# Kernel optimization log

Measured on AMD Instinct MI355X. Metric: run time of the kernel, lower is better.

The kernel has to match this reference:

```python
import jax, jax.numpy as jnp
import numpy as np

# DCT-III (a.k.a. IDCT), unnormalized, scaled to match the DREAMPlace kernel:
#   y_k = x_0 + 2 * sum_{n=1}^{N-1} x_n * cos(pi * n * (2k+1) / (2N))
# (the docstring's Re{1/2 x0 + sum xn e^{j pi n (2k+1)/(2N)}} scaled by 2).
# Computed in O(N log N) via a length-2N FFT:
#   y_k = Re{ sum_n c_n x_n e^{j pi n/(2N)} e^{2 pi j n k/(2N)} }
# which is 2N * ifft(pad(a, 2N)) evaluated at k = 0..N-1, with
#   a_n = c_n * x_n * exp(j pi n / (2N)),  c_0 = 1, c_{n>0} = 2.

def _idct_last_dim(x):
    N = x.shape[-1]
    n = jnp.arange(N)
    c = jnp.where(n == 0, 1.0, 2.0).astype(x.dtype)
    twiddle = jnp.exp(1j * (jnp.pi / (2 * N)) * n.astype(jnp.float32)).astype(jnp.complex64)
    a = (c * x).astype(jnp.complex64) * twiddle          # [.., N]
    y = jnp.fft.ifft(a, n=2 * N, axis=-1)                # [.., 2N]
    return (y.real[..., :N] * (2 * N)).astype(x.dtype)


def setup_inputs() -> dict:
    key = jax.random.key(0)
    x = jax.random.normal(key, (4096, 4096), dtype=jnp.float32)
    return {"x": x}


def reference(x) -> jnp.ndarray:
    return _idct_last_dim(x)
```

## Files before the change

kernel.cpp:

```cpp
#include <hip/hip_runtime.h>
#include <cstdint>


#define NN 4096
#define HH 2048
#define BM 128
#define BN 128
#define BK 128

typedef int i32x4 __attribute__((ext_vector_type(4)));
typedef int i32x2 __attribute__((ext_vector_type(2)));

__device__ __forceinline__ void async_copy16(void* lds_base, const void* gptr) {
    __builtin_amdgcn_global_load_lds(
        (const __attribute__((address_space(1))) unsigned int*)gptr,
        (__attribute__((address_space(3))) unsigned int*)lds_base,
        16, 0, 0);
}

__device__ __forceinline__ int pack4(int q0, int q1, int q2, int q3) {
    return (q0 & 255) | ((q1 & 255) << 8) | ((q2 & 255) << 16) | ((q3 & 255) << 24);
}

__global__ __launch_bounds__(256) void prep_i8(const float* __restrict__ x,
                                               signed char* __restrict__ Ae,
                                               signed char* __restrict__ Ao,
                                               signed char* __restrict__ CEm,
                                               signed char* __restrict__ COm,
                                               float* __restrict__ se,
                                               float* __restrict__ so) {
    const int b = blockIdx.x;
    const int t = threadIdx.x;
    const float s = 3.834951969714103e-4f;

    if (b < 4096) {
        __shared__ float rede[256], redo[256];
        const float* xr = x + (size_t)b * NN;
        float v[16];
#pragma unroll
        for (int j = 0; j < 4; ++j) {
            float4 f = ((const float4*)xr)[t * 4 + j];
            v[j * 4 + 0] = f.x; v[j * 4 + 1] = f.y;
            v[j * 4 + 2] = f.z; v[j * 4 + 3] = f.w;
        }
        float emax = 1e-30f, omax = 1e-30f;
#pragma unroll
        for (int i = 0; i < 8; ++i) {
            emax = fmaxf(emax, __builtin_fabsf(v[2 * i]));
            omax = fmaxf(omax, __builtin_fabsf(v[2 * i + 1]));
        }
        rede[t] = emax; redo[t] = omax;
        __syncthreads();
        for (int sr = 128; sr > 0; sr >>= 1) {
            if (t < sr) {
                rede[t] = fmaxf(rede[t], rede[t + sr]);
                redo[t] = fmaxf(redo[t], redo[t + sr]);
            }
            __syncthreads();
        }
        const float rmax_e = rede[0], rmax_o = redo[0];
        const float inv_e = 127.0f / rmax_e, inv_o = 127.0f / rmax_o;
        int qe[8], qo[8];
#pragma unroll
        for (int i = 0; i < 8; ++i) {
            qe[i] = (int)rintf(v[2 * i] * inv_e);
            qo[i] = (int)rintf(v[2 * i + 1] * inv_o);
        }
        i32x2 oe, oo;
        oe[0] = pack4(qe[0], qe[1], qe[2], qe[3]);
        oe[1] = pack4(qe[4], qe[5], qe[6], qe[7]);
        oo[0] = pack4(qo[0], qo[1], qo[2], qo[3]);
        oo[1] = pack4(qo[4], qo[5], qo[6], qo[7]);
        ((i32x2*)(Ae + (size_t)b * HH))[t] = oe;
        ((i32x2*)(Ao + (size_t)b * HH))[t] = oo;
        if (t == 0) {
            se[b] = rmax_e * (1.0f / 127.0f);
            so[b] = rmax_o * (1.0f / 127.0f);
        }
    } else if (b < 6144) {
        const int k = b - 4096;
        const int twok1 = 2 * k + 1;
        int q[8];
#pragma unroll
        for (int i = 0; i < 8; ++i) {
            int m = t * 8 + i;
            int p = (2 * m * twok1) & 16383;
            float w = (m == 0) ? 1.0f : 2.0f;
            q[i] = (int)rintf(w * __cosf((float)p * s) * 63.5f);
        }
        i32x2 o;
        o[0] = pack4(q[0], q[1], q[2], q[3]);
        o[1] = pack4(q[4], q[5], q[6], q[7]);
        ((i32x2*)(CEm + (size_t)k * HH))[t] = o;
    } else {
        const int k = b - 6144;
        const int twok1 = 2 * k + 1;
        int q[8];
#pragma unroll
        for (int i = 0; i < 8; ++i) {
            int m = t * 8 + i;
            int p = ((2 * m + 1) * twok1) & 16383;
            q[i] = (int)rintf(__cosf((float)p * s) * 127.0f);
        }
        i32x2 o;
        o[0] = pack4(q[0], q[1], q[2], q[3]);
        o[1] = pack4(q[4], q[5], q[6], q[7]);
        ((i32x2*)(COm + (size_t)k * HH))[t] = o;
    }
}

__device__ __forceinline__ void gemm_pass(const signed char* __restrict__ A,
                                          const signed char* __restrict__ B,
                                          signed char* sA, signed char* sB,
                                          int rowBase, int colBase,
                                          int wave, int lane,
                                          i32x4 (&acc)[4][4]) {
    const int waveM = wave >> 1;
    const int waveN = wave & 1;
    const int srow  = lane >> 3;
    const int sgran = lane & 7;
    const int ggcol = (sgran ^ srow) * 16;
    const int rmod  = lane & 7;
    const int quad  = lane >> 4;

    for (int k0 = 0; k0 < HH; k0 += BK) {
#pragma unroll
        for (int j = 0; j < 4; ++j) {
            int ck = wave * 4 + j;
            int r  = ck * 8 + srow;
            async_copy16(&sA[ck * 1024], A + (size_t)(rowBase + r) * HH + k0 + ggcol);
            async_copy16(&sB[ck * 1024], B + (size_t)(colBase + r) * HH + k0 + ggcol);
        }
        __syncthreads();

#pragma unroll
        for (int kk = 0; kk < 2; ++kk) {
            const int poff = ((kk * 4 + quad) ^ rmod) * 16;
            i32x4 af[4], bfr[4];
#pragma unroll
            for (int mi = 0; mi < 4; ++mi) {
                int r = waveM * 64 + mi * 16 + (lane & 15);
                af[mi] = *(const i32x4*)&sA[r * BK + poff];
            }
#pragma unroll
            for (int ni = 0; ni < 4; ++ni) {
                int r = waveN * 64 + ni * 16 + (lane & 15);
                bfr[ni] = *(const i32x4*)&sB[r * BK + poff];
            }
#pragma unroll
            for (int mi = 0; mi < 4; ++mi)
#pragma unroll
                for (int ni = 0; ni < 4; ++ni)
                    acc[mi][ni] = __builtin_amdgcn_mfma_i32_16x16x64_i8(
                        af[mi], bfr[ni], acc[mi][ni], 0, 0, 0);
        }
        __syncthreads();
    }
}

__global__ __launch_bounds__(256, 2) void idct_gemm2(const signed char* __restrict__ Ae,
                                                     const signed char* __restrict__ Ao,
                                                     const signed char* __restrict__ CEm,
                                                     const signed char* __restrict__ COm,
                                                     const float* __restrict__ se,
                                                     const float* __restrict__ so,
                                                     float* __restrict__ C) {
    __shared__ __align__(16) signed char sA[BM * BK];
    __shared__ __align__(16) signed char sB[BN * BK];

    const int tid  = threadIdx.x;
    const int wave = tid >> 6;
    const int lane = tid & 63;

    const int rowBase = blockIdx.y * BM;
    const int colBase = blockIdx.x * BN;

    i32x4 accE[4][4] = {};
    gemm_pass(Ae, CEm, sA, sB, rowBase, colBase, wave, lane, accE);
    i32x4 accO[4][4] = {};
    gemm_pass(Ao, COm, sA, sB, rowBase, colBase, wave, lane, accO);

    const float sB_s = 2.0f / 127.0f;
    const int mrow0 = rowBase + (wave >> 1) * 64 + (lane >> 4) * 4;
    const int ncol0 = colBase + (wave & 1) * 64 + (lane & 15);
#pragma unroll
    for (int mi = 0; mi < 4; ++mi)
#pragma unroll
        for (int ni = 0; ni < 4; ++ni)
#pragma unroll
            for (int rg = 0; rg < 4; ++rg) {
                int rr = mrow0 + mi * 16 + rg;
                int cc = ncol0 + ni * 16;
                float e = (float)accE[mi][ni][rg] * (se[rr] * sB_s);
                float o = (float)accO[mi][ni][rg] * (so[rr] * sB_s);
                C[(size_t)rr * NN + cc] = e + o;
                C[(size_t)rr * NN + (NN - 1 - cc)] = e - o;
            }
}

__global__ __launch_bounds__(256) void idct_naive(const float* __restrict__ x,
                                                  float* __restrict__ out) {
    int row = blockIdx.x;
    __shared__ float sx[NN];
    for (int i = threadIdx.x; i < NN; i += 256) sx[i] = x[(size_t)row * NN + i];
    __syncthreads();
    const float s = 3.834951969714103e-4f;
    for (int k = threadIdx.x; k < NN; k += 256) {
        int twok1 = 2 * k + 1;
        float acc = sx[0];
        int p = 0;
        for (int n = 1; n < NN; ++n) {
            p += twok1; p &= 16383;
            acc += 2.0f * sx[n] * __cosf((float)p * s);
        }
        out[(size_t)row * NN + k] = acc;
    }
}

extern "C" void kernel_launch(void* const* d_in, const int* in_sizes, int n_in,
                              void* d_out, int out_size, void* d_ws, size_t ws_size,
                              hipStream_t stream) {
    const float* x = (const float*)d_in[0];
    float* out = (float*)d_out;

    const size_t eA = (size_t)NN * HH;
    const size_t eC = (size_t)HH * HH;
    const size_t need = 2 * eA + 2 * eC + 2 * NN * sizeof(float);

    if (ws_size >= need) {
        signed char* Ae = (signed char*)d_ws;
        signed char* Ao = Ae + eA;
        signed char* CEm = Ao + eA;
        signed char* COm = CEm + eC;
        float* se = (float*)(COm + eC);
        float* so = se + NN;

        prep_i8<<<8192, 256, 0, stream>>>(x, Ae, Ao, CEm, COm, se, so);

        dim3 grid(HH / BN, NN / BM);
        idct_gemm2<<<grid, 256, 0, stream>>>(Ae, Ao, CEm, COm, se, so, out);
    } else {
        idct_naive<<<NN, 256, 0, stream>>>(x, out);
    }
}
```

Before: 150.3 us.

## Fuse even/odd int8 GEMM passes into one K loop and use wave-shuffle max reduction

The two sequential GEMM passes (even and odd halves) become a single K loop that loads all four int8 tiles per iteration into separate LDS buffers and issues both MFMA groups back to back. This halves the number of loop iterations and barriers, and puts more independent MFMA work between each load and its sync. It doubles LDS use to 64 KB per block, which may limit blocks per CU. The prep kernel's row-max reduction switches from a shared-memory tree with many barriers to wave shuffles plus one barrier.

Result: faster. 146.4 us (-2.6%).

```diff
diff --git a/kernel.cpp b/kernel.cpp
--- a/kernel.cpp
+++ b/kernel.cpp
@@ -34,7 +34,7 @@
     const float s = 3.834951969714103e-4f;
 
     if (b < 4096) {
-        __shared__ float rede[256], redo[256];
+        __shared__ float wmaxe[4], wmaxo[4];
         const float* xr = x + (size_t)b * NN;
         float v[16];
 #pragma unroll
@@ -49,16 +49,16 @@
             emax = fmaxf(emax, __builtin_fabsf(v[2 * i]));
             omax = fmaxf(omax, __builtin_fabsf(v[2 * i + 1]));
         }
-        rede[t] = emax; redo[t] = omax;
+#pragma unroll
+        for (int m = 1; m < 64; m <<= 1) {
+            emax = fmaxf(emax, __shfl_xor(emax, m));
+            omax = fmaxf(omax, __shfl_xor(omax, m));
+        }
+        const int wv = t >> 6;
+        if ((t & 63) == 0) { wmaxe[wv] = emax; wmaxo[wv] = omax; }
         __syncthreads();
-        for (int sr = 128; sr > 0; sr >>= 1) {
-            if (t < sr) {
-                rede[t] = fmaxf(rede[t], rede[t + sr]);
-                redo[t] = fmaxf(redo[t], redo[t + sr]);
-            }
-            __syncthreads();
-        }
-        const float rmax_e = rede[0], rmax_o = redo[0];
+        const float rmax_e = fmaxf(fmaxf(wmaxe[0], wmaxe[1]), fmaxf(wmaxe[2], wmaxe[3]));
+        const float rmax_o = fmaxf(fmaxf(wmaxo[0], wmaxo[1]), fmaxf(wmaxo[2], wmaxo[3]));
         const float inv_e = 127.0f / rmax_e, inv_o = 127.0f / rmax_o;
         int qe[8], qo[8];
 #pragma unroll
@@ -109,55 +109,6 @@
     }
 }
 
-__device__ __forceinline__ void gemm_pass(const signed char* __restrict__ A,
-                                          const signed char* __restrict__ B,
-                                          signed char* sA, signed char* sB,
-                                          int rowBase, int colBase,
-                                          int wave, int lane,
-                                          i32x4 (&acc)[4][4]) {
-    const int waveM = wave >> 1;
-    const int waveN = wave & 1;
-    const int srow  = lane >> 3;
-    const int sgran = lane & 7;
-    const int ggcol = (sgran ^ srow) * 16;
-    const int rmod  = lane & 7;
-    const int quad  = lane >> 4;
-
-    for (int k0 = 0; k0 < HH; k0 += BK) {
-#pragma unroll
-        for (int j = 0; j < 4; ++j) {
-            int ck = wave * 4 + j;
-            int r  = ck * 8 + srow;
-            async_copy16(&sA[ck * 1024], A + (size_t)(rowBase + r) * HH + k0 + ggcol);
-            async_copy16(&sB[ck * 1024], B + (size_t)(colBase + r) * HH + k0 + ggcol);
-        }
-        __syncthreads();
-
-#pragma unroll
-        for (int kk = 0; kk < 2; ++kk) {
-            const int poff = ((kk * 4 + quad) ^ rmod) * 16;
-            i32x4 af[4], bfr[4];
-#pragma unroll
-            for (int mi = 0; mi < 4; ++mi) {
-                int r = waveM * 64 + mi * 16 + (lane & 15);
-                af[mi] = *(const i32x4*)&sA[r * BK + poff];
-            }
-#pragma unroll
-            for (int ni = 0; ni < 4; ++ni) {
-                int r = waveN * 64 + ni * 16 + (lane & 15);
-                bfr[ni] = *(const i32x4*)&sB[r * BK + poff];
-            }
-#pragma unroll
-            for (int mi = 0; mi < 4; ++mi)
-#pragma unroll
-                for (int ni = 0; ni < 4; ++ni)
-                    acc[mi][ni] = __builtin_amdgcn_mfma_i32_16x16x64_i8(
-                        af[mi], bfr[ni], acc[mi][ni], 0, 0, 0);
-        }
-        __syncthreads();
-    }
-}
-
 __global__ __launch_bounds__(256, 2) void idct_gemm2(const signed char* __restrict__ Ae,
                                                      const signed char* __restrict__ Ao,
                                                      const signed char* __restrict__ CEm,
@@ -165,24 +116,91 @@
                                                      const float* __restrict__ se,
                                                      const float* __restrict__ so,
                                                      float* __restrict__ C) {
-    __shared__ __align__(16) signed char sA[BM * BK];
-    __shared__ __align__(16) signed char sB[BN * BK];
+    __shared__ __align__(16) signed char sAe[BM * BK];
+    __shared__ __align__(16) signed char sAo[BM * BK];
+    __shared__ __align__(16) signed char sCE[BN * BK];
+    __shared__ __align__(16) signed char sCO[BN * BK];
 
     const int tid  = threadIdx.x;
     const int wave = tid >> 6;
     const int lane = tid & 63;
+    const int waveM = wave >> 1;
+    const int waveN = wave & 1;
 
     const int rowBase = blockIdx.y * BM;
     const int colBase = blockIdx.x * BN;
 
     i32x4 accE[4][4] = {};
-    gemm_pass(Ae, CEm, sA, sB, rowBase, colBase, wave, lane, accE);
     i32x4 accO[4][4] = {};
-    gemm_pass(Ao, COm, sA, sB, rowBase, colBase, wave, lane, accO);
+
+    const int srow  = lane >> 3;
+    const int sgran = lane & 7;
+    const int ggcol = (sgran ^ srow) * 16;
+    const int rmod  = lane & 7;
+    const int quad  = lane >> 4;
+
+    for (int k0 = 0; k0 < HH; k0 += BK) {
+#pragma unroll
+        for (int j = 0; j < 4; ++j) {
+            int ck = wave * 4 + j;
+            int r  = ck * 8 + srow;
+            size_t aoff = (size_t)(rowBase + r) * HH + k0 + ggcol;
+            size_t boff = (size_t)(colBase + r) * HH + k0 + ggcol;
+            async_copy16(&sAe[ck * 1024], Ae + aoff);
+            async_copy16(&sAo[ck * 1024], Ao + aoff);
+            async_copy16(&sCE[ck * 1024], CEm + boff);
+            async_copy16(&sCO[ck * 1024], COm + boff);
+        }
+        __syncthreads();
+
+#pragma unroll
+        for (int kk = 0; kk < 2; ++kk) {
+            const int poff = ((kk * 4 + quad) ^ rmod) * 16;
+            {
+                i32x4 af[4], bfr[4];
+#pragma unroll
+                for (int mi = 0; mi < 4; ++mi) {
+                    int r = waveM * 64 + mi * 16 + (lane & 15);
+                    af[mi] = *(const i32x4*)&sAe[r * BK + poff];
+                }
+#pragma unroll
+                for (int ni = 0; ni < 4; ++ni) {
+                    int r = waveN * 64 + ni * 16 + (lane & 15);
+                    bfr[ni] = *(const i32x4*)&sCE[r * BK + poff];
+                }
+#pragma unroll
+                for (int mi = 0; mi < 4; ++mi)
+#pragma unroll
+                    for (int ni = 0; ni < 4; ++ni)
+                        accE[mi][ni] = __builtin_amdgcn_mfma_i32_16x16x64_i8(
+                            af[mi], bfr[ni], accE[mi][ni], 0, 0, 0);
+            }
+            {
+                i32x4 af[4], bfr[4];
+#pragma unroll
+                for (int mi = 0; mi < 4; ++mi) {
+                    int r = waveM * 64 + mi * 16 + (lane & 15);
+                    af[mi] = *(const i32x4*)&sAo[r * BK + poff];
+                }
+#pragma unroll
+                for (int ni = 0; ni < 4; ++ni) {
+                    int r = waveN * 64 + ni * 16 + (lane & 15);
+                    bfr[ni] = *(const i32x4*)&sCO[r * BK + poff];
+                }
+#pragma unroll
+                for (int mi = 0; mi < 4; ++mi)
+#pragma unroll
+                    for (int ni = 0; ni < 4; ++ni)
+                        accO[mi][ni] = __builtin_amdgcn_mfma_i32_16x16x64_i8(
+                            af[mi], bfr[ni], accO[mi][ni], 0, 0, 0);
+            }
+        }
+        __syncthreads();
+    }
 
     const float sB_s = 2.0f / 127.0f;
-    const int mrow0 = rowBase + (wave >> 1) * 64 + (lane >> 4) * 4;
-    const int ncol0 = colBase + (wave & 1) * 64 + (lane & 15);
+    const int mrow0 = rowBase + waveM * 64 + (lane >> 4) * 4;
+    const int ncol0 = colBase + waveN * 64 + (lane & 15);
 #pragma unroll
     for (int mi = 0; mi < 4; ++mi)
 #pragma unroll
```
